# Optimization experiments

Hardware: AMD Instinct MI355X
Metric: run time of the kernel (lower is better)

## Reference

```python
import jax, jax.numpy as jnp
import numpy as np

NUM_HEADS = 16


def setup_inputs() -> dict:
    key = jax.random.key(0)
    k1, k2, k3 = jax.random.split(key, 3)
    T, B, E = 2048, 2, 1024
    query = jax.random.normal(k1, (T, B, E), dtype=jnp.float32)
    # xavier-uniform-ish init for qkv weight, small normal for output proj
    lim = (6.0 / (3 * E + E)) ** 0.5
    W_qkv = jax.random.uniform(k2, (3 * E, E), dtype=jnp.float32, minval=-lim, maxval=lim)
    W_o = jax.random.normal(k3, (E, E), dtype=jnp.float32) * 0.02
    b_qkv = jnp.zeros((3 * E,), dtype=jnp.float32)
    b_o = jnp.zeros((E,), dtype=jnp.float32)
    return {"query": query, "W_qkv": W_qkv, "b_qkv": b_qkv, "W_o": W_o, "b_o": b_o}


def reference(query, W_qkv, b_qkv, W_o, b_o):
    T, B, E = query.shape
    H = NUM_HEADS
    hd = E // H
    scaling = float(hd) ** -0.5

    # fused qkv projection: [T, B, 3E]
    qkv = jnp.einsum('tbe,fe->tbf', query, W_qkv) + b_qkv
    q, k, v = jnp.split(qkv, 3, axis=-1)
    q = q * scaling

    def to_heads(x):  # [T, B, E] -> [B*H, T, hd]
        return x.reshape(T, B * H, hd).transpose(1, 0, 2)

    q, k, v = to_heads(q), to_heads(k), to_heads(v)

    # explicit bmm QK^T -> softmax -> bmm AV (faithful to source)
    scores = jnp.einsum('bqd,bkd->bqk', q, k)          # [B*H, T, T]
    attn = jax.nn.softmax(scores, axis=-1)             # dropout p=0.0 (eval)
    ctx = jnp.einsum('bqk,bkd->bqd', attn, v)          # [B*H, T, hd]

    out = ctx.transpose(1, 0, 2).reshape(T, B, E)
    out = jnp.einsum('tbe,fe->tbf', out, W_o) + b_o    # o_net

    avg_weights = attn.reshape(B, H, T, T).sum(axis=1) / H  # need_weights=True path
    return out, avg_weights
```

## Files before the change

kernel.cpp:

```cpp
#include <hip/hip_runtime.h>
#include <stdint.h>

typedef unsigned short u16;
typedef __bf16 bf16x8 __attribute__((ext_vector_type(8)));
typedef float f32x4 __attribute__((ext_vector_type(4)));
typedef float f32x16 __attribute__((ext_vector_type(16)));

__device__ __forceinline__ u16 f2b(float f) {
  unsigned u = __builtin_bit_cast(unsigned, f);
  u += 0x7fffu + ((u >> 16) & 1u);
  return (u16)(u >> 16);
}

__device__ __forceinline__ float fexp2(float x) { return __builtin_amdgcn_exp2f(x); }

__device__ __forceinline__ void gld_lds16(const void* g, void* l) {
  __builtin_amdgcn_global_load_lds((const __attribute__((address_space(1))) unsigned int*)g,
                                   (__attribute__((address_space(3))) unsigned int*)l,
                                   16, 0, 0);
}

__global__ __launch_bounds__(256) void k_cvt(const float* __restrict__ s,
                                             u16* __restrict__ d, int n4) {
  int i = blockIdx.x * 256 + threadIdx.x;
  if (i >= n4) return;
  float4 v = reinterpret_cast<const float4*>(s)[i];
  ushort4 o;
  o.x = f2b(v.x); o.y = f2b(v.y); o.z = f2b(v.z); o.w = f2b(v.w);
  reinterpret_cast<ushort4*>(d)[i] = o;
}

template <int EPI>
__global__ __launch_bounds__(256) void k_gemm_nt(
    const u16* __restrict__ A, const u16* __restrict__ B, const float* __restrict__ bias,
    float* __restrict__ outF, u16* __restrict__ q_ws, u16* __restrict__ k_ws,
    u16* __restrict__ vt_ws) {
  __shared__ u16 Al[2][4096];
  __shared__ u16 Bl[2][4096];
  const int tid = threadIdx.x;
  const int w = tid >> 6, lane = tid & 63;
  const int wr = w >> 1, wc = w & 1;
  const int lo = lane & 15, hi = lane >> 4;
  const int tm = blockIdx.y, tn = blockIdx.x;
  const size_t arow0 = (size_t)tm * 128;
  const size_t brow0 = (size_t)tn * 128;

  f32x4 acc[4][4] = {};

  const int rr = lane >> 2;
  const int kc = (lane & 3) * 8;

  {
    const int k0 = kc;
    for (int rs = 0; rs < 2; ++rs) {
      int seg = rs * 4 + w;
      gld_lds16(A + (arow0 + seg * 16 + rr) * 1024 + k0, &Al[0][seg * 512 + lane * 8]);
      gld_lds16(B + (brow0 + seg * 16 + rr) * 1024 + k0, &Bl[0][seg * 512 + lane * 8]);
    }
  }
  __syncthreads();
  int cur = 0;
  for (int kb = 0; kb < 32; ++kb) {
    if (kb + 1 < 32) {
      const int k0 = (kb + 1) * 32 + kc;
      for (int rs = 0; rs < 2; ++rs) {
        int seg = rs * 4 + w;
        gld_lds16(A + (arow0 + seg * 16 + rr) * 1024 + k0, &Al[cur ^ 1][seg * 512 + lane * 8]);
        gld_lds16(B + (brow0 + seg * 16 + rr) * 1024 + k0, &Bl[cur ^ 1][seg * 512 + lane * 8]);
      }
    }
    bf16x8 af[4], bfr[4];
#pragma unroll
    for (int m = 0; m < 4; ++m)
      af[m] = *(const bf16x8*)&Al[cur][(wr * 64 + m * 16 + lo) * 32 + hi * 8];
#pragma unroll
    for (int n = 0; n < 4; ++n)
      bfr[n] = *(const bf16x8*)&Bl[cur][(wc * 64 + n * 16 + lo) * 32 + hi * 8];
#pragma unroll
    for (int m = 0; m < 4; ++m)
#pragma unroll
      for (int n = 0; n < 4; ++n)
        acc[m][n] = __builtin_amdgcn_mfma_f32_16x16x32_bf16(af[m], bfr[n], acc[m][n], 0, 0, 0);
    __syncthreads();
    cur ^= 1;
  }

  if (EPI == 0) {
#pragma unroll
    for (int n = 0; n < 4; ++n) {
      const int col = tn * 128 + wc * 64 + n * 16 + lo;
      const float bb = bias[col];
#pragma unroll
      for (int m = 0; m < 4; ++m)
#pragma unroll
        for (int r = 0; r < 4; ++r) {
          const int row = tm * 128 + wr * 64 + m * 16 + hi * 4 + r;
          outF[(size_t)row * 1024 + col] = acc[m][n][r] + bb;
        }
    }
  } else {
    const int sec = tn >> 3;
#pragma unroll
    for (int n = 0; n < 4; ++n) {
      const int cin = (tn & 7) * 128 + wc * 64 + n * 16 + lo;
      const int h = cin >> 6, d = cin & 63;
      const float bb = bias[sec * 1024 + cin];
#pragma unroll
      for (int m = 0; m < 4; ++m) {
        const int rowb = tm * 128 + wr * 64 + m * 16 + hi * 4;
        const int t0 = rowb >> 1;
        const float v0 = acc[m][n][0] + bb, v1 = acc[m][n][1] + bb;
        const float v2 = acc[m][n][2] + bb, v3 = acc[m][n][3] + bb;
        if (sec == 0) {
          const float s = 0.18033688f;
          q_ws[(((size_t)h * 2048 + t0) * 64) + d]            = f2b(v0 * s);
          q_ws[(((size_t)(16 + h) * 2048 + t0) * 64) + d]     = f2b(v1 * s);
          q_ws[(((size_t)h * 2048 + t0 + 1) * 64) + d]        = f2b(v2 * s);
          q_ws[(((size_t)(16 + h) * 2048 + t0 + 1) * 64) + d] = f2b(v3 * s);
        } else if (sec == 1) {
          k_ws[(((size_t)h * 2048 + t0) * 64) + d]            = f2b(v0);
          k_ws[(((size_t)(16 + h) * 2048 + t0) * 64) + d]     = f2b(v1);
          k_ws[(((size_t)h * 2048 + t0 + 1) * 64) + d]        = f2b(v2);
          k_ws[(((size_t)(16 + h) * 2048 + t0 + 1) * 64) + d] = f2b(v3);
        } else {
          const int tp0 = (t0 & ~12) | ((t0 & 4) << 1) | ((t0 & 8) >> 1);
          ushort2 p0, p1;
          p0.x = f2b(v0); p0.y = f2b(v2);
          p1.x = f2b(v1); p1.y = f2b(v3);
          *(ushort2*)(vt_ws + ((size_t)h * 64 + d) * 2048 + tp0) = p0;
          *(ushort2*)(vt_ws + ((size_t)(16 + h) * 64 + d) * 2048 + tp0) = p1;
        }
      }
    }
  }
}

__global__ __launch_bounds__(256) void k_flash(
    const u16* __restrict__ q_ws, const u16* __restrict__ k_ws, const u16* __restrict__ vt_ws,
    u16* __restrict__ ctx_ws, float* __restrict__ c_ws) {
  __shared__ __align__(16) u16 KVl[2][8192];
  const int tid = threadIdx.x, w = tid >> 6, lane = tid & 63;
  const int h = lane >> 5, l31 = lane & 31, l7 = lane & 7;

  const int flat = blockIdx.y * 16 + blockIdx.x;
  const int xcd = flat & 7, slot = flat >> 3;
  const int bh = xcd * 4 + (slot >> 4);
  const int qtile = slot & 15;
  const int b = bh >> 4, head = bh & 15;
  const int qbase = qtile * 128;
  const int qrow = qbase + w * 32 + l31;

  bf16x8 qf[4];
#pragma unroll
  for (int j = 0; j < 4; ++j)
    qf[j] = *(const bf16x8*)(q_ws + ((size_t)bh * 2048 + qrow) * 64 + j * 16 + h * 8);

  const int srow = tid >> 3, schk = tid & 7;
  const int xc = (schk ^ (srow & 7)) * 8;
  const u16* kgA = k_ws + ((size_t)bh * 2048 + srow) * 64 + xc;
  const u16* vgA = vt_ws + ((size_t)bh * 64 + srow) * 2048 + xc;

  f32x16 ca0 = {}, ca1 = {};
  float lrow = 0.f;

  {
    u16* base = (u16*)KVl;
    gld_lds16(kgA,             base + tid * 8);
    gld_lds16(kgA + 32 * 64,   base + 2048 + tid * 8);
    gld_lds16(vgA,             base + 4096 + tid * 8);
    gld_lds16(vgA + 32 * 2048, base + 6144 + tid * 8);
  }
  __syncthreads();

  int cur = 0;
  for (int kt = 0; kt < 32; ++kt) {
    if (kt < 31) {
      u16* base = (u16*)KVl + (cur ^ 1) * 8192;
      const u16* kgt = kgA + (size_t)(kt + 1) * 4096;
      const u16* vgt = vgA + (kt + 1) * 64;
      gld_lds16(kgt,             base + tid * 8);
      gld_lds16(kgt + 32 * 64,   base + 2048 + tid * 8);
      gld_lds16(vgt,             base + 4096 + tid * 8);
      gld_lds16(vgt + 32 * 2048, base + 6144 + tid * 8);
    }
    const char* Kb = (const char*)KVl + cur * 16384;
    const char* Vb = Kb + 8192;

    f32x16 st0 = {}, st1 = {};
    __builtin_amdgcn_s_setprio(1);
#pragma unroll
    for (int j = 0; j < 4; ++j) {
      bf16x8 k0 = *(const bf16x8*)(Kb + l31 * 128 + (((2 * j + h) ^ l7) * 16));
      bf16x8 k1 = *(const bf16x8*)(Kb + (32 + l31) * 128 + (((2 * j + h) ^ l7) * 16));
      st0 = __builtin_amdgcn_mfma_f32_32x32x16_bf16(k0, qf[j], st0, 0, 0, 0);
      st1 = __builtin_amdgcn_mfma_f32_32x32x16_bf16(k1, qf[j], st1, 0, 0, 0);
    }
    __builtin_amdgcn_s_setprio(0);

    float ps0 = 0.f, ps1 = 0.f;
#pragma unroll
    for (int r = 0; r < 16; ++r) { float p = fexp2(st0[r]); st0[r] = p; ps0 += p; }
#pragma unroll
    for (int r = 0; r < 16; ++r) { float p = fexp2(st1[r]); st1[r] = p; ps1 += p; }
    float ps = ps0 + ps1;
    ps += __shfl_xor(ps, 32, 64);
    lrow += ps;

    bf16x8 pb00, pb01, pb10, pb11;
#pragma unroll
    for (int i = 0; i < 8; ++i) {
      pb00[i] = (__bf16)st0[i];
      pb01[i] = (__bf16)st0[8 + i];
      pb10[i] = (__bf16)st1[i];
      pb11[i] = (__bf16)st1[8 + i];
    }

    __builtin_amdgcn_s_setprio(1);
#pragma unroll
    for (int t2 = 0; t2 < 2; ++t2)
#pragma unroll
      for (int kp = 0; kp < 2; ++kp) {
        const int ch = (4 * t2 + 2 * kp + h) ^ l7;
        bf16x8 v0 = *(const bf16x8*)(Vb + l31 * 128 + ch * 16);
        bf16x8 v1 = *(const bf16x8*)(Vb + (32 + l31) * 128 + ch * 16);
        const bf16x8 pv = (t2 == 0) ? (kp == 0 ? pb00 : pb01) : (kp == 0 ? pb10 : pb11);
        ca0 = __builtin_amdgcn_mfma_f32_32x32x16_bf16(v0, pv, ca0, 0, 0, 0);
        ca1 = __builtin_amdgcn_mfma_f32_32x32x16_bf16(v1, pv, ca1, 0, 0, 0);
      }
    __builtin_amdgcn_s_setprio(0);

    __syncthreads();
    cur ^= 1;
  }

  const float inv = 1.0f / lrow;
  if (lane < 32) {
    c_ws[(size_t)bh * 2048 + qrow] = inv;
  }

  u16* tw = (u16*)KVl + w * 2048;
#pragma unroll
  for (int r = 0; r < 16; ++r) {
    const int d0 = (r & 3) + 8 * (r >> 2) + 4 * h;
    const int d1 = 32 + d0;
    *(u16*)((char*)tw + l31 * 128 + ((2 * d0) ^ (l7 << 4))) = f2b(ca0[r] * inv);
    *(u16*)((char*)tw + l31 * 128 + ((2 * d1) ^ (l7 << 4))) = f2b(ca1[r] * inv);
  }
  __syncthreads();
#pragma unroll
  for (int it = 0; it < 4; ++it) {
    const int row = it * 8 + (lane >> 3);
    uint4 val = *(const uint4*)((const char*)tw + row * 128 + (((lane & 7) ^ (row & 7)) * 16));
    const int q = qbase + w * 32 + row;
    *(uint4*)(ctx_ws + ((size_t)(q * 2 + b)) * 1024 + head * 64 + (lane & 7) * 8) = val;
  }
}

__global__ __launch_bounds__(256) void k_avg(
    const u16* __restrict__ q_ws, const u16* __restrict__ k_ws,
    const float* __restrict__ c_ws, float* __restrict__ avg) {
  __shared__ __align__(16) u16 Kl[2][128 * 64];
  const int tid = threadIdx.x, w = tid >> 6, lane = tid & 63;
  const int lo = lane & 15, hi = lane >> 4;
  const int kbase = blockIdx.x * 128;
  const int qb = blockIdx.y * 64;
  const int b = blockIdx.z;
  const int qrow = qb + w * 16 + lo;
  const int qrow_base = qb + w * 16 + hi * 4;

  const int r0 = tid >> 3, c0 = tid & 7;
  const int ldsoff = r0 * 128 + ((c0 ^ (r0 & 7)) << 4);
  const u16* kg = k_ws + ((size_t)(b * 16) * 2048 + kbase + r0) * 64 + c0 * 8;
  const int l7 = lo & 7;

  float acc[8][4] = {};
  const f32x4 zero = {0.f, 0.f, 0.f, 0.f};

  uint4 rg0 = *(const uint4*)(kg);
  uint4 rg1 = *(const uint4*)(kg + 32 * 64);
  uint4 rg2 = *(const uint4*)(kg + 64 * 64);
  uint4 rg3 = *(const uint4*)(kg + 96 * 64);
  {
    char* dst = (char*)Kl[0] + ldsoff;
    *(uint4*)(dst) = rg0;
    *(uint4*)(dst + 32 * 128) = rg1;
    *(uint4*)(dst + 64 * 128) = rg2;
    *(uint4*)(dst + 96 * 128) = rg3;
  }
  __syncthreads();

  int cur = 0;
  for (int h = 0; h < 16; ++h) {
    const int bh = b * 16 + h;
    if (h + 1 < 16) {
      const u16* kgn = kg + (size_t)(h + 1) * 2048 * 64;
      rg0 = *(const uint4*)(kgn);
      rg1 = *(const uint4*)(kgn + 32 * 64);
      rg2 = *(const uint4*)(kgn + 64 * 64);
      rg3 = *(const uint4*)(kgn + 96 * 64);
    }
    const u16* qp = q_ws + ((size_t)bh * 2048 + qrow) * 64 + hi * 8;
    bf16x8 qf0 = *(const bf16x8*)qp;
    bf16x8 qf1 = *(const bf16x8*)(qp + 32);
    const float4 cf = *(const float4*)(c_ws + (size_t)bh * 2048 + qrow_base);
    const float cfa[4] = {cf.x, cf.y, cf.z, cf.w};
    const char* kbse = (const char*)Kl[cur];
#pragma unroll
    for (int n = 0; n < 8; ++n) {
      const char* kp = kbse + (n * 16 + lo) * 128;
      bf16x8 k0 = *(const bf16x8*)(kp + ((hi ^ l7) << 4));
      bf16x8 k1 = *(const bf16x8*)(kp + (((hi + 4) ^ l7) << 4));
      f32x4 s = __builtin_amdgcn_mfma_f32_16x16x32_bf16(qf0, k0, zero, 0, 0, 0);
      s = __builtin_amdgcn_mfma_f32_16x16x32_bf16(qf1, k1, s, 0, 0, 0);
#pragma unroll
      for (int r = 0; r < 4; ++r) acc[n][r] += fexp2(s[r]) * cfa[r];
    }
    if (h + 1 < 16) {
      char* dst = (char*)Kl[cur ^ 1] + ldsoff;
      *(uint4*)(dst) = rg0;
      *(uint4*)(dst + 32 * 128) = rg1;
      *(uint4*)(dst + 64 * 128) = rg2;
      *(uint4*)(dst + 96 * 128) = rg3;
      __syncthreads();
    }
    cur ^= 1;
  }

  const float s16 = 1.0f / 16.0f;
#pragma unroll
  for (int n = 0; n < 8; ++n)
#pragma unroll
    for (int r = 0; r < 4; ++r)
      avg[((size_t)(b * 2048 + qrow_base + r)) * 2048 + kbase + n * 16 + lo] = acc[n][r] * s16;
}

extern "C" void kernel_launch(void* const* d_in, const int* in_sizes, int n_in,
                              void* d_out, int out_size, void* d_ws, size_t ws_size,
                              hipStream_t stream) {
  const float* query = (const float*)d_in[0];
  const float* Wqkv  = (const float*)d_in[1];
  const float* bqkv  = (const float*)d_in[2];
  const float* Wo    = (const float*)d_in[3];
  const float* bo    = (const float*)d_in[4];
  float* out = (float*)d_out;
  float* avg = out + (size_t)4096 * 1024;

  char* ws = (char*)d_ws;
  u16* qbf    = (u16*)(ws);
  u16* ctx_ws = (u16*)(ws);
  u16*   wqkvbf = (u16*)(ws + 8388608);
  float* c_ws   = (float*)(ws + 8388608);
  u16* wobf  = (u16*)(ws + 14680064);
  u16* q_ws  = (u16*)(ws + 16777216);
  u16* k_ws  = (u16*)(ws + 25165824);
  u16* vt_ws = (u16*)(ws + 33554432);

  k_cvt<<<dim3(4096), dim3(256), 0, stream>>>(query, qbf, 1048576);
  k_cvt<<<dim3(3072), dim3(256), 0, stream>>>(Wqkv, wqkvbf, 786432);
  k_cvt<<<dim3(1024), dim3(256), 0, stream>>>(Wo, wobf, 262144);
  k_gemm_nt<1><<<dim3(24, 32), dim3(256), 0, stream>>>(
      qbf, wqkvbf, bqkv, nullptr, q_ws, k_ws, vt_ws);
  k_flash<<<dim3(16, 32), dim3(256), 0, stream>>>(
      q_ws, k_ws, vt_ws, ctx_ws, c_ws);
  k_avg<<<dim3(16, 32, 2), dim3(256), 0, stream>>>(
      q_ws, k_ws, c_ws, avg);
  k_gemm_nt<0><<<dim3(8, 32), dim3(256), 0, stream>>>(
      ctx_ws, wobf, bo, out, nullptr, nullptr, nullptr);
}
```

Baseline: 163.8 us.

## Split key range across two wave groups in flash kernel with LDS reduction

Doubles the flash-attention block to 512 threads. Two groups of four waves each stream half of the key/value sequence into their own double-buffered LDS region, so each runs half as many iterations. At the end, the second group writes its partial context accumulators and row sums to LDS, and the first group adds them before normalizing and storing. The aim is more waves in flight per CU to hide latency, at the cost of a larger LDS footprint and an extra LDS reduction pass.

```diff
diff --git a/kernel.cpp b/kernel.cpp
--- a/kernel.cpp
+++ b/kernel.cpp
@@ -135,12 +135,15 @@
   }
 }
 
-__global__ __launch_bounds__(256) void k_flash(
+__global__ __launch_bounds__(512) void k_flash(
     const u16* __restrict__ q_ws, const u16* __restrict__ k_ws, const u16* __restrict__ vt_ws,
     u16* __restrict__ ctx_ws, float* __restrict__ c_ws) {
-  __shared__ __align__(16) u16 KVl[2][8192];
+  __shared__ __align__(16) u16 KVl[32768];
   const int tid = threadIdx.x, w = tid >> 6, lane = tid & 63;
   const int h = lane >> 5, l31 = lane & 31, l7 = lane & 7;
+  const int hh = w >> 2;
+  const int wq = w & 3;
+  const int tid_h = tid & 255;
 
   const int flat = blockIdx.y * 16 + blockIdx.x;
   const int xcd = flat & 7, slot = flat >> 3;
@@ -148,42 +151,42 @@
   const int qtile = slot & 15;
   const int b = bh >> 4, head = bh & 15;
   const int qbase = qtile * 128;
-  const int qrow = qbase + w * 32 + l31;
+  const int qrow = qbase + wq * 32 + l31;
 
   bf16x8 qf[4];
 #pragma unroll
   for (int j = 0; j < 4; ++j)
     qf[j] = *(const bf16x8*)(q_ws + ((size_t)bh * 2048 + qrow) * 64 + j * 16 + h * 8);
 
-  const int srow = tid >> 3, schk = tid & 7;
+  const int srow = tid_h >> 3, schk = tid_h & 7;
   const int xc = (schk ^ (srow & 7)) * 8;
-  const u16* kgA = k_ws + ((size_t)bh * 2048 + srow) * 64 + xc;
-  const u16* vgA = vt_ws + ((size_t)bh * 64 + srow) * 2048 + xc;
+  const u16* kgA = k_ws + ((size_t)bh * 2048 + hh * 16 * 64 + srow) * 64 + xc;
+  const u16* vgA = vt_ws + ((size_t)bh * 64 + srow) * 2048 + hh * 16 * 64 + xc;
 
   f32x16 ca0 = {}, ca1 = {};
   float lrow = 0.f;
 
   {
-    u16* base = (u16*)KVl;
-    gld_lds16(kgA,             base + tid * 8);
-    gld_lds16(kgA + 32 * 64,   base + 2048 + tid * 8);
-    gld_lds16(vgA,             base + 4096 + tid * 8);
-    gld_lds16(vgA + 32 * 2048, base + 6144 + tid * 8);
+    u16* base = KVl + hh * 8192;
+    gld_lds16(kgA,             base + tid_h * 8);
+    gld_lds16(kgA + 32 * 64,   base + 2048 + tid_h * 8);
+    gld_lds16(vgA,             base + 4096 + tid_h * 8);
+    gld_lds16(vgA + 32 * 2048, base + 6144 + tid_h * 8);
   }
   __syncthreads();
 
   int cur = 0;
-  for (int kt = 0; kt < 32; ++kt) {
-    if (kt < 31) {
-      u16* base = (u16*)KVl + (cur ^ 1) * 8192;
-      const u16* kgt = kgA + (size_t)(kt + 1) * 4096;
-      const u16* vgt = vgA + (kt + 1) * 64;
-      gld_lds16(kgt,             base + tid * 8);
-      gld_lds16(kgt + 32 * 64,   base + 2048 + tid * 8);
-      gld_lds16(vgt,             base + 4096 + tid * 8);
-      gld_lds16(vgt + 32 * 2048, base + 6144 + tid * 8);
-    }
-    const char* Kb = (const char*)KVl + cur * 16384;
+  for (int it = 0; it < 16; ++it) {
+    if (it < 15) {
+      u16* base = KVl + (cur ^ 1) * 16384 + hh * 8192;
+      const u16* kgt = kgA + (size_t)(it + 1) * 4096;
+      const u16* vgt = vgA + (it + 1) * 64;
+      gld_lds16(kgt,             base + tid_h * 8);
+      gld_lds16(kgt + 32 * 64,   base + 2048 + tid_h * 8);
+      gld_lds16(vgt,             base + 4096 + tid_h * 8);
+      gld_lds16(vgt + 32 * 2048, base + 6144 + tid_h * 8);
+    }
+    const char* Kb = (const char*)(KVl + cur * 16384 + hh * 8192);
     const char* Vb = Kb + 8192;
 
     f32x16 st0 = {}, st1 = {};
@@ -233,26 +236,44 @@
     cur ^= 1;
   }
 
-  const float inv = 1.0f / lrow;
-  if (lane < 32) {
-    c_ws[(size_t)bh * 2048 + qrow] = inv;
-  }
-
-  u16* tw = (u16*)KVl + w * 2048;
-#pragma unroll
-  for (int r = 0; r < 16; ++r) {
-    const int d0 = (r & 3) + 8 * (r >> 2) + 4 * h;
-    const int d1 = 32 + d0;
-    *(u16*)((char*)tw + l31 * 128 + ((2 * d0) ^ (l7 << 4))) = f2b(ca0[r] * inv);
-    *(u16*)((char*)tw + l31 * 128 + ((2 * d1) ^ (l7 << 4))) = f2b(ca1[r] * inv);
-  }
-  __syncthreads();
-#pragma unroll
-  for (int it = 0; it < 4; ++it) {
-    const int row = it * 8 + (lane >> 3);
-    uint4 val = *(const uint4*)((const char*)tw + row * 128 + (((lane & 7) ^ (row & 7)) * 16));
-    const int q = qbase + w * 32 + row;
-    *(uint4*)(ctx_ws + ((size_t)(q * 2 + b)) * 1024 + head * 64 + (lane & 7) * 8) = val;
+  float* F = (float*)KVl;
+  if (w >= 4) {
+    const int g = w - 4;
+#pragma unroll
+    for (int r = 0; r < 16; ++r) {
+      F[g * 2048 + r * 64 + lane] = ca0[r];
+      F[g * 2048 + (16 + r) * 64 + lane] = ca1[r];
+    }
+    F[8192 + g * 64 + lane] = lrow;
+  }
+  __syncthreads();
+  u16* tw = (u16*)((char*)KVl + 34816 + w * 4096);
+  if (w < 4) {
+#pragma unroll
+    for (int r = 0; r < 16; ++r) {
+      ca0[r] += F[w * 2048 + r * 64 + lane];
+      ca1[r] += F[w * 2048 + (16 + r) * 64 + lane];
+    }
+    lrow += F[8192 + w * 64 + lane];
+    const float inv = 1.0f / lrow;
+    if (lane < 32) c_ws[(size_t)bh * 2048 + qrow] = inv;
+#pragma unroll
+    for (int r = 0; r < 16; ++r) {
+      const int d0 = (r & 3) + 8 * (r >> 2) + 4 * h;
+      const int d1 = 32 + d0;
+      *(u16*)((char*)tw + l31 * 128 + ((2 * d0) ^ (l7 << 4))) = f2b(ca0[r] * inv);
+      *(u16*)((char*)tw + l31 * 128 + ((2 * d1) ^ (l7 << 4))) = f2b(ca1[r] * inv);
+    }
+  }
+  __syncthreads();
+  if (w < 4) {
+#pragma unroll
+    for (int it = 0; it < 4; ++it) {
+      const int row = it * 8 + (lane >> 3);
+      uint4 val = *(const uint4*)((const char*)tw + row * 128 + (((lane & 7) ^ (row & 7)) * 16));
+      const int q = qbase + wq * 32 + row;
+      *(uint4*)(ctx_ws + ((size_t)(q * 2 + b)) * 1024 + head * 64 + (lane & 7) * 8) = val;
+    }
   }
 }
 
@@ -360,7 +381,7 @@
   k_cvt<<<dim3(1024), dim3(256), 0, stream>>>(Wo, wobf, 262144);
   k_gemm_nt<1><<<dim3(24, 32), dim3(256), 0, stream>>>(
       qbf, wqkvbf, bqkv, nullptr, q_ws, k_ws, vt_ws);
-  k_flash<<<dim3(16, 32), dim3(256), 0, stream>>>(
+  k_flash<<<dim3(16, 32), dim3(512), 0, stream>>>(
       q_ws, k_ws, vt_ws, ctx_ws, c_ws);
   k_avg<<<dim3(16, 32, 2), dim3(256), 0, stream>>>(
       q_ws, k_ws, c_ws, avg);
```

New measurement: 157.4 us. 1.04x faster.
